# Performance work log

Hardware: AMD Instinct MI355X
Metric: run time of the kernel (lower is better)

Reference implementation:

```python
import jax, jax.numpy as jnp
import numpy as np

N = 50000
E = 800000
IN_DIM = 128
HIDDEN = 32
HEADS = 4
NUM_CLASSES = 10


def _glorot(key, shape):
    fan_in, fan_out = shape
    lim = float(np.sqrt(6.0 / (fan_in + fan_out)))
    return jax.random.uniform(key, shape, jnp.float32, -lim, lim)


def transformer_conv(x, src, dst, Wq, bq, Wk, bk, Wv, bv, Ws, bs, heads, out_ch, concat):
    """PyG TransformerConv (root_weight=True, beta=False, no edge_attr), eval mode."""
    n = x.shape[0]
    q = (x @ Wq + bq).reshape(n, heads, out_ch)
    k = (x @ Wk + bk).reshape(n, heads, out_ch)
    v = (x @ Wv + bv).reshape(n, heads, out_ch)
    # gather per-edge: query from target i, key/value from source j
    qe = q[dst]                                  # [E, H, C]
    ke = k[src]                                  # [E, H, C]
    ve = v[src]                                  # [E, H, C]
    logits = jnp.einsum('ehc,ehc->eh', qe, ke) / jnp.sqrt(jnp.float32(out_ch))
    # segment softmax over incoming edges of each target node
    m = jax.ops.segment_max(logits, dst, num_segments=n)        # [N, H]
    m = jnp.where(jnp.isfinite(m), m, 0.0)
    e = jnp.exp(logits - m[dst])                                # [E, H]
    denom = jax.ops.segment_sum(e, dst, num_segments=n)         # [N, H]
    alpha = e / (denom[dst] + 1e-16)                            # [E, H]
    agg = jax.ops.segment_sum(alpha[..., None] * ve, dst, num_segments=n)  # [N, H, C]
    if concat:
        out = agg.reshape(n, heads * out_ch)
    else:
        out = agg.mean(axis=1)
    return out + x @ Ws + bs  # root/skip connection


def setup_inputs() -> dict:
    key = jax.random.key(0)
    ks = jax.random.split(key, 20)
    x = jax.random.normal(ks[0], (N, IN_DIM), jnp.float32)
    edge_index = jax.random.randint(ks[1], (2, E), 0, N, jnp.int32)
    d1 = HEADS * HIDDEN  # conv1 per-head stacked width = 128
    params = {
        'Wq1': _glorot(ks[2], (IN_DIM, d1)), 'bq1': jnp.zeros((d1,), jnp.float32),
        'Wk1': _glorot(ks[3], (IN_DIM, d1)), 'bk1': jnp.zeros((d1,), jnp.float32),
        'Wv1': _glorot(ks[4], (IN_DIM, d1)), 'bv1': jnp.zeros((d1,), jnp.float32),
        'Ws1': _glorot(ks[5], (IN_DIM, d1)), 'bs1': jnp.zeros((d1,), jnp.float32),
        'Wq2': _glorot(ks[6], (d1, NUM_CLASSES)), 'bq2': jnp.zeros((NUM_CLASSES,), jnp.float32),
        'Wk2': _glorot(ks[7], (d1, NUM_CLASSES)), 'bk2': jnp.zeros((NUM_CLASSES,), jnp.float32),
        'Wv2': _glorot(ks[8], (d1, NUM_CLASSES)), 'bv2': jnp.zeros((NUM_CLASSES,), jnp.float32),
        'Ws2': _glorot(ks[9], (d1, NUM_CLASSES)), 'bs2': jnp.zeros((NUM_CLASSES,), jnp.float32),
    }
    return {'x': x, 'edge_index': edge_index, **params}


def reference(x, edge_index,
              Wq1, bq1, Wk1, bk1, Wv1, bv1, Ws1, bs1,
              Wq2, bq2, Wk2, bk2, Wv2, bv2, Ws2, bs2):
    src, dst = edge_index[0], edge_index[1]
    h = transformer_conv(x, src, dst, Wq1, bq1, Wk1, bk1, Wv1, bv1, Ws1, bs1,
                         HEADS, HIDDEN, concat=True)
    h = jax.nn.elu(h)
    # dropout is identity in eval mode
    out = transformer_conv(h, src, dst, Wq2, bq2, Wk2, bk2, Wv2, bv2, Ws2, bs2,
                           1, NUM_CLASSES, concat=False)
    return out
```

## Files before the change

kernel.cpp:

```cpp
#include <hip/hip_runtime.h>
#include <hip/hip_fp16.h>
#include <math.h>

#define NN 50000
#define EE 800000
#define NB 196
#define NBK 128
#define BKN 391
#define CH 4096

typedef _Float16 f16x8 __attribute__((ext_vector_type(8)));
typedef float f32x4 __attribute__((ext_vector_type(4)));
typedef float f32x2 __attribute__((ext_vector_type(2)));

__device__ inline float elu1(float x) { return x > 0.f ? x : expm1f(x); }

__global__ __launch_bounds__(256) void convert_x_deg(
    const float* __restrict__ x, __half* __restrict__ xh,
    const int* __restrict__ dst, int* __restrict__ deg)
{
    const int i = blockIdx.x * 256 + threadIdx.x;
    if (i < NN * 32) {
        const float4 v = ((const float4*)x)[i];
        ((__half2*)xh)[i * 2] = __floats2half2_rn(v.x, v.y);
        ((__half2*)xh)[i * 2 + 1] = __floats2half2_rn(v.z, v.w);
    }
    if (i < EE) atomicAdd(&deg[dst[i]], 1);
}

__global__ __launch_bounds__(256) void build_weights(
    const float* __restrict__ Wq, const float* __restrict__ Wk,
    const float* __restrict__ Wv, const float* __restrict__ Ws,
    const float* __restrict__ Wq2, const float* __restrict__ bq2,
    const float* __restrict__ Wk2, const float* __restrict__ bk2,
    const float* __restrict__ Wv2, const float* __restrict__ bv2,
    const float* __restrict__ Ws2, const float* __restrict__ bs2,
    __half* __restrict__ Wt, __half* __restrict__ W2t, float* __restrict__ bias2)
{
    const int idx = blockIdx.x * 256 + threadIdx.x;
    if (idx < 8192) {
        const int col = idx >> 7, k = idx & 127;
        const int m = col >> 4, j = col & 15;
        const float* W = m == 0 ? Wq2 : m == 1 ? Wk2 : m == 2 ? Wv2 : Ws2;
        W2t[idx] = (__half)(j < 10 ? W[k * 10 + j] : 0.f);
    }
    if (idx < 64) {
        const int m = idx >> 4, j = idx & 15;
        const float* b = m == 0 ? bq2 : m == 1 ? bk2 : m == 2 ? bv2 : bs2;
        bias2[idx] = j < 10 ? b[j] : 0.f;
    }
    __shared__ float tile[32][33];
    const int mat = blockIdx.x >> 4;
    const int tid = blockIdx.x & 15;
    const int k0 = (tid >> 2) * 32, c0 = (tid & 3) * 32;
    const float* W = mat == 0 ? Wq : mat == 1 ? Wk : mat == 2 ? Wv : Ws;
    const int r = threadIdx.x >> 5;
    const int c = threadIdx.x & 31;
    for (int rr = r; rr < 32; rr += 8) tile[rr][c] = W[(size_t)(k0 + rr) * 128 + c0 + c];
    __syncthreads();
    for (int rr = r; rr < 32; rr += 8)
        Wt[((size_t)mat * 128 + c0 + rr) * 128 + k0 + c] = (__half)tile[c][rr];
}

__global__ __launch_bounds__(256) void block_sums(
    const int* __restrict__ deg, int* __restrict__ bsum)
{
    __shared__ int ws[4];
    const int t = threadIdx.x;
    const int idx = blockIdx.x * 256 + t;
    int d = (idx < NN) ? deg[idx] : 0;
    #pragma unroll
    for (int off = 32; off; off >>= 1) d += __shfl_down(d, off, 64);
    if ((t & 63) == 0) ws[t >> 6] = d;
    __syncthreads();
    if (t == 0) bsum[blockIdx.x] = ws[0] + ws[1] + ws[2] + ws[3];
}

__global__ __launch_bounds__(256) void scan_bsums(int* __restrict__ bsum)
{
    __shared__ int s[256];
    const int t = threadIdx.x;
    int v = (t < NB) ? bsum[t] : 0;
    s[t] = v;
    __syncthreads();
    for (int off = 1; off < 256; off <<= 1) {
        int u = (t >= off) ? s[t - off] : 0;
        __syncthreads();
        s[t] += u;
        __syncthreads();
    }
    if (t < NB) bsum[t] = (t == 0) ? 0 : s[t - 1];
}

__global__ __launch_bounds__(256) void write_rowptr(
    const int* __restrict__ deg, const int* __restrict__ bsum,
    int* __restrict__ rowptr, int* __restrict__ bcur)
{
    __shared__ int s[256];
    const int t = threadIdx.x;
    const int idx = blockIdx.x * 256 + t;
    const int d = (idx < NN) ? deg[idx] : 0;
    s[t] = d;
    __syncthreads();
    for (int off = 1; off < 256; off <<= 1) {
        int u = (t >= off) ? s[t - off] : 0;
        __syncthreads();
        s[t] += u;
        __syncthreads();
    }
    const int excl = ((t == 0) ? 0 : s[t - 1]) + bsum[blockIdx.x];
    if (idx < NN) {
        rowptr[idx] = excl;
        if (idx % BKN == 0) bcur[idx / BKN] = excl;
    }
    if (idx == NN - 1) rowptr[NN] = excl + d;
}

__global__ __launch_bounds__(256) void bucket_stage(
    const int* __restrict__ src, const int* __restrict__ dst,
    int* __restrict__ bcur, unsigned* __restrict__ bpair)
{
    __shared__ unsigned ep[CH];
    __shared__ unsigned short eb[CH];
    __shared__ unsigned stg[CH];
    __shared__ int cnt[NBK], off[NBK], pos[NBK], gbase[NBK];
    const int t = threadIdx.x;
    const int e0 = blockIdx.x * CH;
    const int n = min(CH, EE - e0);
    if (t < NBK) cnt[t] = 0;
    __syncthreads();
    for (int i = t; i < n; i += 256) {
        const int s = src[e0 + i], d = dst[e0 + i];
        ep[i] = (unsigned)s | ((unsigned)d << 16);
        const int b = d / BKN;
        eb[i] = (unsigned short)b;
        atomicAdd(&cnt[b], 1);
    }
    __syncthreads();
    if (t == 0) {
        int run = 0;
        for (int b = 0; b < NBK; ++b) { off[b] = run; pos[b] = run; run += cnt[b]; }
    }
    __syncthreads();
    if (t < NBK && cnt[t] > 0) gbase[t] = atomicAdd(&bcur[t], cnt[t]);
    __syncthreads();
    for (int i = t; i < n; i += 256) {
        const int b = eb[i];
        const int p = atomicAdd(&pos[b], 1);
        stg[p] = ep[i];
    }
    __syncthreads();
    for (int i = t; i < n; i += 256) {
        int lo = 0, hi = NBK - 1;
        while (lo < hi) { const int mid = (lo + hi + 1) >> 1; if (off[mid] <= i) lo = mid; else hi = mid - 1; }
        bpair[gbase[lo] + (i - off[lo])] = stg[i];
    }
}

__global__ __launch_bounds__(256) void bucket_scatter(
    const unsigned* __restrict__ bpair, const int* __restrict__ rowptr,
    int* __restrict__ esrc)
{
    __shared__ int lcur[BKN];
    const int b = blockIdx.x;
    const int n0 = b * BKN;
    const int n1 = min(NN, n0 + BKN);
    const int nn = n1 - n0;
    const int t = threadIdx.x;
    for (int i = t; i < nn; i += 256) lcur[i] = rowptr[n0 + i];
    __syncthreads();
    const int ebeg = rowptr[n0];
    const int eend = rowptr[n1];
    for (int i = ebeg + t; i < eend; i += 256) {
        const unsigned p = bpair[i];
        const int s = (int)(p & 0xFFFFu);
        const int d = (int)(p >> 16);
        const int pos = atomicAdd(&lcur[d - n0], 1);
        esrc[pos] = s;
    }
}

__global__ __launch_bounds__(128) void gemm_l1_mfma(
    const __half* __restrict__ xh, const __half* __restrict__ Wt,
    const float* __restrict__ bq, const float* __restrict__ bk,
    const float* __restrict__ bv, const float* __restrict__ bs,
    __half* __restrict__ oqh, unsigned char* __restrict__ ok8,
    unsigned char* __restrict__ ov8, __half* __restrict__ osh)
{
    __shared__ __align__(16) unsigned char ldsraw[128 * 272];
    const int pair = blockIdx.y;
    const int t = threadIdx.x;
    const int wave = t >> 6;
    const int lane = t & 63;
    const int l = lane & 15;
    const int g = lane >> 4;
    const int brow0 = blockIdx.x * 128;
    const int wrow0 = brow0 + wave * 64;

    f16x8 xf[4][4];
    #pragma unroll
    for (int rt = 0; rt < 4; ++rt) {
        int arow = wrow0 + rt * 16 + l;
        if (arow >= NN) arow = NN - 1;
        #pragma unroll
        for (int kk = 0; kk < 4; ++kk)
            xf[rt][kk] = *(const f16x8*)((const _Float16*)xh + (size_t)arow * 128 + kk * 32 + g * 8);
    }

    for (int mi = 0; mi < 2; ++mi) {
        const int mat = pair * 2 + mi;
        const bool isfp8 = (mat == 1 || mat == 2);
        const float* b = mat == 0 ? bq : mat == 1 ? bk : mat == 2 ? bv : bs;
        const _Float16* wt = (const _Float16*)Wt + (size_t)mat * 128 * 128;

        f16x8 wf[4], wfn[4];
        #pragma unroll
        for (int kk = 0; kk < 4; ++kk)
            wf[kk] = *(const f16x8*)(wt + (size_t)l * 128 + kk * 32 + g * 8);

        for (int ct = 0; ct < 8; ++ct) {
            if (ct < 7) {
                const int ncol = (ct + 1) * 16 + l;
                #pragma unroll
                for (int kk = 0; kk < 4; ++kk)
                    wfn[kk] = *(const f16x8*)(wt + (size_t)ncol * 128 + kk * 32 + g * 8);
            }
            f32x4 acc[4];
            #pragma unroll
            for (int rt = 0; rt < 4; ++rt) acc[rt] = (f32x4){0.f, 0.f, 0.f, 0.f};
            #pragma unroll
            for (int kk = 0; kk < 4; ++kk)
                #pragma unroll
                for (int rt = 0; rt < 4; ++rt)
                    acc[rt] = __builtin_amdgcn_mfma_f32_16x16x32_f16(wf[kk], xf[rt][kk], acc[rt], 0, 0, 0);

            const int col0 = ct * 16 + g * 4;
            const float4 bias = *(const float4*)(b + col0);
            #pragma unroll
            for (int rt = 0; rt < 4; ++rt) {
                const int lrow = wave * 64 + rt * 16 + l;
                const float r0 = acc[rt][0] + bias.x;
                const float r1 = acc[rt][1] + bias.y;
                const float r2 = acc[rt][2] + bias.z;
                const float r3 = acc[rt][3] + bias.w;
                if (isfp8) {
                    int p = __builtin_amdgcn_cvt_pk_fp8_f32(r0, r1, 0, false);
                    p = __builtin_amdgcn_cvt_pk_fp8_f32(r2, r3, p, true);
                    *(int*)&ldsraw[lrow * 144 + col0] = p;
                } else {
                    __half2 h01 = __floats2half2_rn(r0, r1);
                    __half2 h23 = __floats2half2_rn(r2, r3);
                    uint2 u;
                    u.x = *(unsigned*)&h01;
                    u.y = *(unsigned*)&h23;
                    *(uint2*)&ldsraw[lrow * 272 + col0 * 2] = u;
                }
            }
            #pragma unroll
            for (int kk = 0; kk < 4; ++kk) wf[kk] = wfn[kk];
        }

        __syncthreads();
        if (isfp8) {
            unsigned char* o = (mat == 1) ? ok8 : ov8;
            #pragma unroll
            for (int i = 0; i < 8; ++i) {
                const int idx = i * 128 + t;
                const int row = idx >> 3;
                const int seg = idx & 7;
                const int grow = brow0 + row;
                if (grow < NN)
                    *(uint4*)(o + (size_t)grow * 128 + seg * 16) = *(const uint4*)&ldsraw[row * 144 + seg * 16];
            }
        } else {
            __half* o = (mat == 0) ? oqh : osh;
            #pragma unroll
            for (int i = 0; i < 16; ++i) {
                const int idx = i * 128 + t;
                const int row = idx >> 4;
                const int seg = idx & 15;
                const int grow = brow0 + row;
                if (grow < NN)
                    *(uint4*)(o + (size_t)grow * 128 + seg * 8) = *(const uint4*)&ldsraw[row * 272 + seg * 16];
            }
        }
        __syncthreads();
    }
}

__global__ __launch_bounds__(256) void node_attn1(
    const __half* __restrict__ q1, const unsigned char* __restrict__ k8,
    const unsigned char* __restrict__ v8,
    const int* __restrict__ rowptr, const int* __restrict__ esrc,
    const __half* __restrict__ skiph,
    __half* __restrict__ hb)
{
    const int t = threadIdx.x;
    const int d = blockIdx.x * 8 + (t >> 5);
    if (d >= NN) return;
    const int ch4 = (t & 31) << 2;

    const int beg = rowptr[d];
    const int end = rowptr[d + 1];

    float q0, q1v, q2, q3;
    {
        const __half2 qa = *(const __half2*)(q1 + (size_t)d * 128 + ch4);
        const __half2 qb = *(const __half2*)(q1 + (size_t)d * 128 + ch4 + 2);
        const float2 fa = __half22float2(qa);
        const float2 fb = __half22float2(qb);
        q0 = fa.x * 0.17677669529663687f;
        q1v = fa.y * 0.17677669529663687f;
        q2 = fb.x * 0.17677669529663687f;
        q3 = fb.y * 0.17677669529663687f;
    }

    f32x4 accA = {0.f, 0.f, 0.f, 0.f}, accB = {0.f, 0.f, 0.f, 0.f};
    float sA = 0.f, sB = 0.f;

    int i = beg;
    int sa = (i < end) ? esrc[i] : 0;
    int sb = (i + 1 < end) ? esrc[i + 1] : 0;
    unsigned kA = *(const unsigned*)(k8 + (size_t)sa * 128 + ch4);
    unsigned vA = *(const unsigned*)(v8 + (size_t)sa * 128 + ch4);
    unsigned kB = *(const unsigned*)(k8 + (size_t)sb * 128 + ch4);
    unsigned vB = *(const unsigned*)(v8 + (size_t)sb * 128 + ch4);

    while (i + 1 < end) {
        const int ni = i + 2;
        const int nsa = (ni < end) ? esrc[ni] : 0;
        const int nsb = (ni + 1 < end) ? esrc[ni + 1] : 0;
        const unsigned nkA = *(const unsigned*)(k8 + (size_t)nsa * 128 + ch4);
        const unsigned nvA = *(const unsigned*)(v8 + (size_t)nsa * 128 + ch4);
        const unsigned nkB = *(const unsigned*)(k8 + (size_t)nsb * 128 + ch4);
        const unsigned nvB = *(const unsigned*)(v8 + (size_t)nsb * 128 + ch4);

        const f32x2 kA01 = __builtin_amdgcn_cvt_pk_f32_fp8((int)kA, false);
        const f32x2 kA23 = __builtin_amdgcn_cvt_pk_f32_fp8((int)kA, true);
        const f32x2 kB01 = __builtin_amdgcn_cvt_pk_f32_fp8((int)kB, false);
        const f32x2 kB23 = __builtin_amdgcn_cvt_pk_f32_fp8((int)kB, true);

        float pA = q0 * kA01[0] + q1v * kA01[1] + q2 * kA23[0] + q3 * kA23[1];
        float pB = q0 * kB01[0] + q1v * kB01[1] + q2 * kB23[0] + q3 * kB23[1];
        pA += __shfl_xor(pA, 4, 8); pB += __shfl_xor(pB, 4, 8);
        pA += __shfl_xor(pA, 2, 8); pB += __shfl_xor(pB, 2, 8);
        pA += __shfl_xor(pA, 1, 8); pB += __shfl_xor(pB, 1, 8);

        const f32x2 vA01 = __builtin_amdgcn_cvt_pk_f32_fp8((int)vA, false);
        const f32x2 vA23 = __builtin_amdgcn_cvt_pk_f32_fp8((int)vA, true);
        const f32x2 vB01 = __builtin_amdgcn_cvt_pk_f32_fp8((int)vB, false);
        const f32x2 vB23 = __builtin_amdgcn_cvt_pk_f32_fp8((int)vB, true);

        const float exA = __expf(pA - 4.0f);
        accA[0] += exA * vA01[0];
        accA[1] += exA * vA01[1];
        accA[2] += exA * vA23[0];
        accA[3] += exA * vA23[1];
        sA += exA;

        const float exB = __expf(pB - 4.0f);
        accB[0] += exB * vB01[0];
        accB[1] += exB * vB01[1];
        accB[2] += exB * vB23[0];
        accB[3] += exB * vB23[1];
        sB += exB;

        kA = nkA; vA = nvA; kB = nkB; vB = nvB;
        i = ni;
    }
    if (i < end) {
        const f32x2 kA01 = __builtin_amdgcn_cvt_pk_f32_fp8((int)kA, false);
        const f32x2 kA23 = __builtin_amdgcn_cvt_pk_f32_fp8((int)kA, true);
        float pA = q0 * kA01[0] + q1v * kA01[1] + q2 * kA23[0] + q3 * kA23[1];
        pA += __shfl_xor(pA, 4, 8);
        pA += __shfl_xor(pA, 2, 8);
        pA += __shfl_xor(pA, 1, 8);
        const f32x2 vA01 = __builtin_amdgcn_cvt_pk_f32_fp8((int)vA, false);
        const f32x2 vA23 = __builtin_amdgcn_cvt_pk_f32_fp8((int)vA, true);
        const float exA = __expf(pA - 4.0f);
        accA[0] += exA * vA01[0];
        accA[1] += exA * vA01[1];
        accA[2] += exA * vA23[0];
        accA[3] += exA * vA23[1];
        sA += exA;
    }

    const float inv = 1.f / (sA + sB + 1e-16f);
    const __half2 sk01 = *(const __half2*)(skiph + (size_t)d * 128 + ch4);
    const __half2 sk23 = *(const __half2*)(skiph + (size_t)d * 128 + ch4 + 2);
    const float2 s01 = __half22float2(sk01);
    const float2 s23 = __half22float2(sk23);
    const float o0 = elu1(s01.x + (accA[0] + accB[0]) * inv);
    const float o1 = elu1(s01.y + (accA[1] + accB[1]) * inv);
    const float o2 = elu1(s23.x + (accA[2] + accB[2]) * inv);
    const float o3 = elu1(s23.y + (accA[3] + accB[3]) * inv);
    __half2 h01 = __floats2half2_rn(o0, o1);
    __half2 h23 = __floats2half2_rn(o2, o3);
    uint2 u;
    u.x = *(unsigned*)&h01;
    u.y = *(unsigned*)&h23;
    *(uint2*)(hb + (size_t)d * 128 + ch4) = u;
}

__global__ __launch_bounds__(128) void node_l2_mfma(
    const __half* __restrict__ hb, const __half* __restrict__ W2t,
    const float* __restrict__ bias2,
    __half* __restrict__ q2h, __half* __restrict__ kv2h,
    float* __restrict__ out)
{
    const int t = threadIdx.x;
    const int wave = t >> 6;
    const int lane = t & 63;
    const int l = lane & 15;
    const int g = lane >> 4;
    const int wrow0 = blockIdx.x * 128 + wave * 64;
    if (wrow0 >= NN) return;
    const bool full = (wrow0 + 64 <= NN);

    f16x8 hf[4][4];
    #pragma unroll
    for (int rt = 0; rt < 4; ++rt) {
        int arow = wrow0 + rt * 16 + l;
        if (!full && arow >= NN) arow = NN - 1;
        #pragma unroll
        for (int kk = 0; kk < 4; ++kk)
            hf[rt][kk] = *(const f16x8*)((const _Float16*)hb + (size_t)arow * 128 + kk * 32 + g * 8);
    }

    #pragma unroll
    for (int ct = 0; ct < 4; ++ct) {
        const int col = ct * 16 + l;
        f16x8 wf[4];
        #pragma unroll
        for (int kk = 0; kk < 4; ++kk)
            wf[kk] = *(const f16x8*)((const _Float16*)W2t + (size_t)col * 128 + kk * 32 + g * 8);

        f32x4 acc[4];
        #pragma unroll
        for (int rt = 0; rt < 4; ++rt) acc[rt] = (f32x4){0.f, 0.f, 0.f, 0.f};
        #pragma unroll
        for (int kk = 0; kk < 4; ++kk)
            #pragma unroll
            for (int rt = 0; rt < 4; ++rt)
                acc[rt] = __builtin_amdgcn_mfma_f32_16x16x32_f16(wf[kk], hf[rt][kk], acc[rt], 0, 0, 0);

        const int c0 = g * 4;
        const float4 bias = *(const float4*)(bias2 + ct * 16 + c0);
        #pragma unroll
        for (int rt = 0; rt < 4; ++rt) {
            const int row = wrow0 + rt * 16 + l;
            if (full || row < NN) {
                float4 r;
                r.x = acc[rt][0] + bias.x;
                r.y = acc[rt][1] + bias.y;
                r.z = acc[rt][2] + bias.z;
                r.w = acc[rt][3] + bias.w;
                if (ct == 3) {
                    if (g < 2) {
                        *(float2*)(out + (size_t)row * 10 + c0) = make_float2(r.x, r.y);
                        *(float2*)(out + (size_t)row * 10 + c0 + 2) = make_float2(r.z, r.w);
                    } else if (g == 2) {
                        *(float2*)(out + (size_t)row * 10 + 8) = make_float2(r.x, r.y);
                    }
                } else {
                    __half* p = ct == 0 ? q2h + (size_t)row * 16 + c0
                              : kv2h + (size_t)row * 32 + (ct == 2 ? 16 : 0) + c0;
                    __half2 h01 = __floats2half2_rn(r.x, r.y);
                    __half2 h23 = __floats2half2_rn(r.z, r.w);
                    uint2 u;
                    u.x = *(unsigned*)&h01;
                    u.y = *(unsigned*)&h23;
                    *(uint2*)p = u;
                }
            }
        }
    }
}

__global__ __launch_bounds__(256) void node_attn2(
    const __half* __restrict__ q2h, const __half* __restrict__ kv2h,
    const int* __restrict__ rowptr, const int* __restrict__ esrc,
    float* __restrict__ out)
{
    const int t = threadIdx.x;
    const int d = blockIdx.x * 32 + (t >> 3);
    if (d >= NN) return;
    const int c = t & 7;
    const int beg = rowptr[d];
    const int end = rowptr[d + 1];

    float2 qv = __half22float2(*(const __half2*)(q2h + (size_t)d * 16 + 2 * c));
    qv.x *= 0.31622776601683794f;
    qv.y *= 0.31622776601683794f;

    float2 acc[4];
    float ss[4];
    #pragma unroll
    for (int j = 0; j < 4; ++j) { acc[j] = make_float2(0.f, 0.f); ss[j] = 0.f; }

    int i = beg;
    __half2 kr[4], vr[4];
    #pragma unroll
    for (int j = 0; j < 4; ++j) {
        const int s = (i + j < end) ? esrc[i + j] : 0;
        kr[j] = *(const __half2*)(kv2h + (size_t)s * 32 + 2 * c);
        vr[j] = *(const __half2*)(kv2h + (size_t)s * 32 + 16 + 2 * c);
    }

    while (i + 3 < end) {
        const int ni = i + 4;
        __half2 nk[4], nv[4];
        #pragma unroll
        for (int j = 0; j < 4; ++j) {
            const int s = (ni + j < end) ? esrc[ni + j] : 0;
            nk[j] = *(const __half2*)(kv2h + (size_t)s * 32 + 2 * c);
            nv[j] = *(const __half2*)(kv2h + (size_t)s * 32 + 16 + 2 * c);
        }
        #pragma unroll
        for (int j = 0; j < 4; ++j) {
            const float2 kf = __half22float2(kr[j]);
            const float2 vf = __half22float2(vr[j]);
            float p = qv.x * kf.x + qv.y * kf.y;
            p += __shfl_xor(p, 4, 8);
            p += __shfl_xor(p, 2, 8);
            p += __shfl_xor(p, 1, 8);
            const float ex = __expf(p - 2.0f);
            acc[j].x += ex * vf.x;
            acc[j].y += ex * vf.y;
            ss[j] += ex;
        }
        #pragma unroll
        for (int j = 0; j < 4; ++j) { kr[j] = nk[j]; vr[j] = nv[j]; }
        i = ni;
    }
    for (; i < end; ++i) {
        const int s = esrc[i];
        const float2 kf = __half22float2(*(const __half2*)(kv2h + (size_t)s * 32 + 2 * c));
        const float2 vf = __half22float2(*(const __half2*)(kv2h + (size_t)s * 32 + 16 + 2 * c));
        float p = qv.x * kf.x + qv.y * kf.y;
        p += __shfl_xor(p, 4, 8);
        p += __shfl_xor(p, 2, 8);
        p += __shfl_xor(p, 1, 8);
        const float ex = __expf(p - 2.0f);
        acc[0].x += ex * vf.x;
        acc[0].y += ex * vf.y;
        ss[0] += ex;
    }

    if (c < 5) {
        const float ssum = ss[0] + ss[1] + ss[2] + ss[3];
        const float inv = 1.f / (ssum + 1e-16f);
        float2 o = *(float2*)(out + (size_t)d * 10 + 2 * c);
        o.x += (acc[0].x + acc[1].x + acc[2].x + acc[3].x) * inv;
        o.y += (acc[0].y + acc[1].y + acc[2].y + acc[3].y) * inv;
        *(float2*)(out + (size_t)d * 10 + 2 * c) = o;
    }
}

extern "C" void kernel_launch(void* const* d_in, const int* in_sizes, int n_in,
                              void* d_out, int out_size, void* d_ws, size_t ws_size,
                              hipStream_t stream) {
    const float* x   = (const float*)d_in[0];
    const int*   ei  = (const int*)d_in[1];
    const float* Wq1 = (const float*)d_in[2];  const float* bq1 = (const float*)d_in[3];
    const float* Wk1 = (const float*)d_in[4];  const float* bk1 = (const float*)d_in[5];
    const float* Wv1 = (const float*)d_in[6];  const float* bv1 = (const float*)d_in[7];
    const float* Ws1 = (const float*)d_in[8];  const float* bs1 = (const float*)d_in[9];
    const float* Wq2 = (const float*)d_in[10]; const float* bq2 = (const float*)d_in[11];
    const float* Wk2 = (const float*)d_in[12]; const float* bk2 = (const float*)d_in[13];
    const float* Wv2 = (const float*)d_in[14]; const float* bv2 = (const float*)d_in[15];
    const float* Ws2 = (const float*)d_in[16]; const float* bs2 = (const float*)d_in[17];
    float* out = (float*)d_out;

    const int* src = ei;
    const int* dst = ei + EE;

    __half* xh    = (__half*)d_ws;
    __half* q1h   = xh + (size_t)NN * 128;
    __half* skiph = q1h + (size_t)NN * 128;
    __half* hb    = skiph + (size_t)NN * 128;
    unsigned char* k8 = (unsigned char*)(hb + (size_t)NN * 128);
    unsigned char* v8 = k8 + (size_t)NN * 128;
    __half* Wt    = (__half*)(v8 + (size_t)NN * 128);
    __half* W2t   = Wt + 4 * 128 * 128;
    __half* q2h   = W2t + 64 * 128;
    __half* kv2h  = q2h + (size_t)NN * 16;
    float* bias2  = (float*)(kv2h + (size_t)NN * 32);
    int* deg      = (int*)(bias2 + 64);
    int* rowptr   = deg + NN;
    int* bcur     = rowptr + NN + 1;
    int* bsum     = bcur + NBK;
    int* esrc     = bsum + NB;
    unsigned* bpair = (unsigned*)(esrc + EE);

    hipMemsetAsync(deg, 0, (size_t)NN * sizeof(int), stream);
    convert_x_deg<<<(NN * 32 + 255) / 256, 256, 0, stream>>>(x, xh, dst, deg);
    build_weights<<<64, 256, 0, stream>>>(Wq1, Wk1, Wv1, Ws1,
                                          Wq2, bq2, Wk2, bk2, Wv2, bv2, Ws2, bs2,
                                          Wt, W2t, bias2);

    block_sums<<<NB, 256, 0, stream>>>(deg, bsum);
    scan_bsums<<<1, 256, 0, stream>>>(bsum);
    write_rowptr<<<NB, 256, 0, stream>>>(deg, bsum, rowptr, bcur);
    bucket_stage<<<(EE + CH - 1) / CH, 256, 0, stream>>>(src, dst, bcur, bpair);
    bucket_scatter<<<NBK, 256, 0, stream>>>(bpair, rowptr, esrc);

    gemm_l1_mfma<<<dim3((NN + 127) / 128, 2), 128, 0, stream>>>(
        xh, Wt, bq1, bk1, bv1, bs1, q1h, k8, v8, skiph);

    node_attn1<<<(NN + 7) / 8, 256, 0, stream>>>(q1h, k8, v8, rowptr, esrc, skiph, hb);

    node_l2_mfma<<<(NN + 127) / 128, 128, 0, stream>>>(hb, W2t, bias2, q2h, kv2h, out);

    node_attn2<<<(NN + 31) / 32, 256, 0, stream>>>(q2h, kv2h, rowptr, esrc, out);
}
```

Before: 187.4 us.

## Process nodes in degree-sorted order in attention kernels for load balance

Adds a degree histogram, scan, and counting-sort scatter to build a node permutation ordered by in-degree, then has both attention kernels map wavefront slots through this permutation. Nodes with similar edge counts land in the same wave, which reduces divergence and idle lanes in the per-edge loops. The cost is three extra small kernel launches and an indirect perm load. Writes now go to scattered rows, which loses the locality of consecutive node indices.

```diff
diff --git a/kernel.cpp b/kernel.cpp
--- a/kernel.cpp
+++ b/kernel.cpp
@@ -8,6 +8,7 @@
 #define NBK 128
 #define BKN 391
 #define CH 4096
+#define NDB 128
 
 typedef _Float16 f16x8 __attribute__((ext_vector_type(8)));
 typedef float f32x4 __attribute__((ext_vector_type(4)));
@@ -60,6 +61,48 @@
     __syncthreads();
     for (int rr = r; rr < 32; rr += 8)
         Wt[((size_t)mat * 128 + c0 + rr) * 128 + k0 + c] = (__half)tile[c][rr];
+}
+
+__global__ __launch_bounds__(256) void deg_hist(
+    const int* __restrict__ deg, int* __restrict__ dhist)
+{
+    const int i = blockIdx.x * 256 + threadIdx.x;
+    if (i < NN) atomicAdd(&dhist[min(deg[i], NDB - 1)], 1);
+}
+
+__global__ __launch_bounds__(256) void scan_dhist(int* __restrict__ dhist)
+{
+    __shared__ int s[NDB];
+    const int t = threadIdx.x;
+    if (t < NDB) s[t] = dhist[t];
+    __syncthreads();
+    if (t == 0) {
+        int run = 0;
+        for (int b = 0; b < NDB; ++b) { const int c = s[b]; s[b] = run; run += c; }
+    }
+    __syncthreads();
+    if (t < NDB) dhist[t] = s[t];
+}
+
+__global__ __launch_bounds__(256) void perm_scatter(
+    const int* __restrict__ deg, int* __restrict__ dcur, int* __restrict__ perm)
+{
+    __shared__ int cnt[NDB], base[NDB];
+    const int t = threadIdx.x;
+    if (t < NDB) cnt[t] = 0;
+    __syncthreads();
+    const int i = blockIdx.x * 256 + t;
+    int b = -1;
+    if (i < NN) { b = min(deg[i], NDB - 1); atomicAdd(&cnt[b], 1); }
+    __syncthreads();
+    if (t < NDB && cnt[t] > 0) base[t] = atomicAdd(&dcur[t], cnt[t]);
+    __syncthreads();
+    if (t < NDB) cnt[t] = 0;
+    __syncthreads();
+    if (i < NN) {
+        const int off = atomicAdd(&cnt[b], 1);
+        perm[base[b] + off] = i;
+    }
 }
 
 __global__ __launch_bounds__(256) void block_sums(
@@ -292,12 +335,14 @@
     const __half* __restrict__ q1, const unsigned char* __restrict__ k8,
     const unsigned char* __restrict__ v8,
     const int* __restrict__ rowptr, const int* __restrict__ esrc,
+    const int* __restrict__ perm,
     const __half* __restrict__ skiph,
     __half* __restrict__ hb)
 {
     const int t = threadIdx.x;
-    const int d = blockIdx.x * 8 + (t >> 5);
-    if (d >= NN) return;
+    const int idx = blockIdx.x * 8 + (t >> 5);
+    if (idx >= NN) return;
+    const int d = perm[idx];
     const int ch4 = (t & 31) << 2;
 
     const int beg = rowptr[d];
@@ -480,11 +525,13 @@
 __global__ __launch_bounds__(256) void node_attn2(
     const __half* __restrict__ q2h, const __half* __restrict__ kv2h,
     const int* __restrict__ rowptr, const int* __restrict__ esrc,
+    const int* __restrict__ perm,
     float* __restrict__ out)
 {
     const int t = threadIdx.x;
-    const int d = blockIdx.x * 32 + (t >> 3);
-    if (d >= NN) return;
+    const int idx = blockIdx.x * 32 + (t >> 3);
+    if (idx >= NN) return;
+    const int d = perm[idx];
     const int c = t & 7;
     const int beg = rowptr[d];
     const int end = rowptr[d + 1];
@@ -587,17 +634,23 @@
     __half* kv2h  = q2h + (size_t)NN * 16;
     float* bias2  = (float*)(kv2h + (size_t)NN * 32);
     int* deg      = (int*)(bias2 + 64);
-    int* rowptr   = deg + NN;
+    int* dhist    = deg + NN;
+    int* perm     = dhist + NDB;
+    int* rowptr   = perm + NN;
     int* bcur     = rowptr + NN + 1;
     int* bsum     = bcur + NBK;
     int* esrc     = bsum + NB;
     unsigned* bpair = (unsigned*)(esrc + EE);
 
-    hipMemsetAsync(deg, 0, (size_t)NN * sizeof(int), stream);
+    hipMemsetAsync(deg, 0, (size_t)(NN + NDB) * sizeof(int), stream);
     convert_x_deg<<<(NN * 32 + 255) / 256, 256, 0, stream>>>(x, xh, dst, deg);
     build_weights<<<64, 256, 0, stream>>>(Wq1, Wk1, Wv1, Ws1,
                                           Wq2, bq2, Wk2, bk2, Wv2, bv2, Ws2, bs2,
                                           Wt, W2t, bias2);
+
+    deg_hist<<<NB, 256, 0, stream>>>(deg, dhist);
+    scan_dhist<<<1, 256, 0, stream>>>(dhist);
+    perm_scatter<<<NB, 256, 0, stream>>>(deg, dhist, perm);
 
     block_sums<<<NB, 256, 0, stream>>>(deg, bsum);
     scan_bsums<<<1, 256, 0, stream>>>(bsum);
@@ -608,9 +661,9 @@
     gemm_l1_mfma<<<dim3((NN + 127) / 128, 2), 128, 0, stream>>>(
         xh, Wt, bq1, bk1, bv1, bs1, q1h, k8, v8, skiph);
 
-    node_attn1<<<(NN + 7) / 8, 256, 0, stream>>>(q1h, k8, v8, rowptr, esrc, skiph, hb);
+    node_attn1<<<(NN + 7) / 8, 256, 0, stream>>>(q1h, k8, v8, rowptr, esrc, perm, skiph, hb);
 
     node_l2_mfma<<<(NN + 127) / 128, 128, 0, stream>>>(hb, W2t, bias2, q2h, kv2h, out);
 
-    node_attn2<<<(NN + 31) / 32, 256, 0, stream>>>(q2h, kv2h, rowptr, esrc, out);
-}
+    node_attn2<<<(NN + 31) / 32, 256, 0, stream>>>(q2h, kv2h, rowptr, esrc, perm, out);
+}
```

Result: slower. 302.9 us (+61.6%).
